# Optimization experiments

Hardware: AMD Instinct MI355X
Metric: run time of the kernel (lower is better)

Reference implementation:

```python
import jax, jax.numpy as jnp
import numpy as np

N = 50000      # nodes
E = 800000     # edges (avg degree 16)
F_IN = 512
HID = 128
OUT = 40
DROPOUT = 0.5


def setup_inputs() -> dict:
    key = jax.random.key(0)
    ks = jax.random.split(key, 9)
    x = jax.random.normal(ks[0], (N, F_IN), dtype=jnp.float32)
    edge_src = jax.random.randint(ks[1], (E,), 0, N, dtype=jnp.int32)
    edge_dst = jax.random.randint(ks[2], (E,), 0, N, dtype=jnp.int32)
    edge_weight = jax.random.uniform(ks[3], (E,), dtype=jnp.float32)
    # GraphConvolution params (Glorot-ish init like the torch reference)
    s1 = 1.0 / np.sqrt(HID)
    W1 = jax.random.uniform(ks[4], (F_IN, HID), minval=-s1, maxval=s1, dtype=jnp.float32)
    b1 = jax.random.uniform(ks[5], (HID,), minval=-s1, maxval=s1, dtype=jnp.float32)
    s2 = 1.0 / np.sqrt(OUT)
    W2 = jax.random.uniform(ks[6], (HID, OUT), minval=-s2, maxval=s2, dtype=jnp.float32)
    b2 = jax.random.uniform(ks[7], (OUT,), minval=-s2, maxval=s2, dtype=jnp.float32)
    # Pre-sampled dropout mask (training-mode dropout, deterministic reference):
    keep = jax.random.bernoulli(ks[8], 1.0 - DROPOUT, (N, HID))
    drop_mask = keep.astype(jnp.float32) / (1.0 - DROPOUT)
    return {"x": x, "W1": W1, "b1": b1, "W2": W2, "b2": b2,
            "edge_weight": edge_weight, "drop_mask": drop_mask,
            "edge_src": edge_src, "edge_dst": edge_dst}


def spmm(edge_src, edge_dst, edge_weight, h):
    # out[i] = sum_{e: dst_e = i} w_e * h[src_e]   (sparse adj @ h)
    msgs = edge_weight[:, None] * h[edge_src]      # [E, d]
    return jax.ops.segment_sum(msgs, edge_dst, num_segments=N)


def reference(x, W1, b1, W2, b2, edge_weight, drop_mask, edge_src, edge_dst):
    # layer 1: adj @ (x @ W1) + b1, relu, dropout
    h = spmm(edge_src, edge_dst, edge_weight, x @ W1) + b1
    h = jax.nn.relu(h) * drop_mask
    # layer 2: adj @ (h @ W2) + b2
    out = spmm(edge_src, edge_dst, edge_weight, h @ W2) + b2
    return out
```

## Files before the change

### kernel.cpp

```cpp
#include <hip/hip_runtime.h>

#define NN 50000
#define NE 800000
#define FIN 512
#define HID 128
#define NOUT 40
#define H2P 64
#define CAP 64
#define NXS 16
#define GB1 782
#define EPB 2048
#define SB  391
#define MB  782

typedef __bf16 v8bf __attribute__((ext_vector_type(8)));
typedef float  v4f  __attribute__((ext_vector_type(4)));
typedef unsigned short us8 __attribute__((ext_vector_type(8)));
typedef unsigned short us4 __attribute__((ext_vector_type(4)));

static __device__ __forceinline__ unsigned short f2bf(float f) {
  union { float f; unsigned int u; } v; v.f = f;
  unsigned int r = v.u + 0x7FFFu + ((v.u >> 16) & 1u);
  return (unsigned short)(r >> 16);
}
static __device__ __forceinline__ float bf2f(unsigned short s) {
  union { unsigned int u; float f; } v; v.u = ((unsigned int)s) << 16;
  return v.f;
}

__global__ void k_w1t(const float* __restrict__ W1, unsigned short* __restrict__ W1t,
                      int* __restrict__ nxt) {
  int id = blockIdx.x * 256 + threadIdx.x;
  int k = id >> 7;
  int n = id & 127;
  W1t[n * FIN + k] = f2bf(W1[k * HID + n]);
  if (id < NN) nxt[(size_t)id * NXS] = 0;
}

#define BM1 64
#define BK1 64
#define BKP1 72
__global__ __launch_bounds__(256) void k_fused(
    const float* __restrict__ x, const unsigned short* __restrict__ W1t,
    unsigned short* __restrict__ hb0,
    const int* __restrict__ src, const int* __restrict__ dst,
    const float* __restrict__ w, int* __restrict__ nxt,
    unsigned int* __restrict__ bkt,
    const float* __restrict__ mask, unsigned int* __restrict__ mpk) {
  __shared__ unsigned short As[BM1 * BKP1];
  __shared__ unsigned short Bs[HID * BKP1];
  const int t = threadIdx.x;

  if (blockIdx.x >= GB1 + SB) {
    int id = (blockIdx.x - (GB1 + SB)) * 256 + t;
    if (id < NN * 4) {
      int row = id >> 2, seg = id & 3;
      const float4* mp = (const float4*)(mask + (size_t)row * HID + seg * 32);
      unsigned int bits = 0;
      #pragma unroll
      for (int q = 0; q < 8; ++q) {
        float4 v = mp[q];
        bits |= (v.x != 0.f ? 1u : 0u) << (q * 4);
        bits |= (v.y != 0.f ? 1u : 0u) << (q * 4 + 1);
        bits |= (v.z != 0.f ? 1u : 0u) << (q * 4 + 2);
        bits |= (v.w != 0.f ? 1u : 0u) << (q * 4 + 3);
      }
      mpk[(size_t)row * 4 + seg] = bits;
    }
    return;
  }

  if (blockIdx.x >= GB1) {
    const int base = (blockIdx.x - GB1) * EPB + t;
    int   ii[8]; unsigned int pk[8]; int ok[8];
    #pragma unroll
    for (int k = 0; k < 8; ++k) {
      int e = base + k * 256;
      ok[k] = (e < NE);
      int ec = ok[k] ? e : (NE - 1);
      ii[k] = dst[ec];
      pk[k] = (unsigned int)src[ec] | ((unsigned int)f2bf(w[ec]) << 16);
    }
    int p[8];
    #pragma unroll
    for (int k = 0; k < 8; ++k)
      p[k] = ok[k] ? atomicAdd(&nxt[(size_t)ii[k] * NXS], 1) : CAP;
    #pragma unroll
    for (int k = 0; k < 8; ++k)
      if (p[k] < CAP) bkt[(size_t)ii[k] * CAP + p[k]] = pk[k];
    return;
  }

  const int r0 = blockIdx.x * BM1;
  const int wave = t >> 6, lane = t & 63;
  const int quad = lane >> 4, mr = lane & 15;
  const int mrow0 = (wave & 1) * 32;
  const int ncol0 = (wave >> 1) * 64;

  const int ar = t >> 2, aq = t & 3;
  int grow = r0 + ar; if (grow > NN - 1) grow = NN - 1;
  const float4* xrow = (const float4*)(x + (size_t)grow * FIN);
  const int bn = t >> 1, bh = t & 1;

  const v4f vzero = {0.f, 0.f, 0.f, 0.f};
  v4f acc[2][4];
  #pragma unroll
  for (int mi = 0; mi < 2; ++mi)
    #pragma unroll
    for (int j = 0; j < 4; ++j) acc[mi][j] = vzero;

  for (int k0 = 0; k0 < FIN; k0 += BK1) {
    float4 va[4];
    #pragma unroll
    for (int i = 0; i < 4; ++i) va[i] = xrow[(k0 >> 2) + aq + i * 4];
    us8 vb[4];
    const us8* bp = (const us8*)(W1t + bn * FIN + k0 + bh * 32);
    #pragma unroll
    for (int i = 0; i < 4; ++i) vb[i] = bp[i];

    __syncthreads();
    #pragma unroll
    for (int i = 0; i < 4; ++i) {
      us4 s; s.x = f2bf(va[i].x); s.y = f2bf(va[i].y);
             s.z = f2bf(va[i].z); s.w = f2bf(va[i].w);
      *(us4*)&As[ar * BKP1 + aq * 4 + i * 16] = s;
    }
    #pragma unroll
    for (int i = 0; i < 4; ++i)
      *(us8*)&Bs[bn * BKP1 + bh * 32 + i * 8] = vb[i];
    __syncthreads();

    #pragma unroll
    for (int ks = 0; ks < BK1; ks += 32) {
      v8bf a0 = *(const v8bf*)&As[(mrow0 + mr) * BKP1 + ks + quad * 8];
      v8bf a1 = *(const v8bf*)&As[(mrow0 + 16 + mr) * BKP1 + ks + quad * 8];
      #pragma unroll
      for (int j = 0; j < 4; ++j) {
        v8bf b = *(const v8bf*)&Bs[(ncol0 + j * 16 + mr) * BKP1 + ks + quad * 8];
        acc[0][j] = __builtin_amdgcn_mfma_f32_16x16x32_bf16(a0, b, acc[0][j], 0, 0, 0);
        acc[1][j] = __builtin_amdgcn_mfma_f32_16x16x32_bf16(a1, b, acc[1][j], 0, 0, 0);
      }
    }
  }

  #pragma unroll
  for (int mi = 0; mi < 2; ++mi)
    #pragma unroll
    for (int j = 0; j < 4; ++j)
      #pragma unroll
      for (int rr = 0; rr < 4; ++rr) {
        int row = r0 + mrow0 + mi * 16 + quad * 4 + rr;
        int col = ncol0 + j * 16 + mr;
        if (row < NN) hb0[(size_t)row * HID + col] = f2bf(acc[mi][j][rr]);
      }
}

__global__ __launch_bounds__(256) void k_spmm1(const unsigned short* __restrict__ hb0,
                                               const int* __restrict__ nxt,
                                               const unsigned int* __restrict__ bkt,
                                               const float* __restrict__ b1,
                                               const unsigned int* __restrict__ mpk,
                                               const float* __restrict__ W2,
                                               unsigned short* __restrict__ h2b) {
  __shared__ unsigned int w2p[64 * NOUT];
  const int t = threadIdx.x, lane = t & 63, wv = t >> 6;
  for (int idx = t; idx < 64 * NOUT; idx += 256) {
    int c2 = idx / NOUT, o = idx - c2 * NOUT;
    w2p[idx] = (unsigned int)f2bf(W2[(2 * c2) * NOUT + o])
             | ((unsigned int)f2bf(W2[(2 * c2 + 1) * NOUT + o]) << 16);
  }
  __syncthreads();

  const int g = lane >> 4, ql = lane & 15;
  const int i = blockIdx.x * 4 + wv;
  const int c0 = ql * 8;
  int nE = nxt[(size_t)i * NXS]; if (nE > CAP) nE = CAP;
  const int m = (nE + 3 - g) >> 2;
  const unsigned int* ep = bkt + (size_t)i * CAP + g;

  float a0[8] = {0.f,0.f,0.f,0.f,0.f,0.f,0.f,0.f};
  float a1[8] = {0.f,0.f,0.f,0.f,0.f,0.f,0.f,0.f};
  int j = 0;
  for (; j + 3 < m; j += 4) {
    unsigned int p0 = ep[4*j], p1 = ep[4*j+4], p2 = ep[4*j+8], p3 = ep[4*j+12];
    int s0 = p0 & 0xFFFF, s1 = p1 & 0xFFFF, s2 = p2 & 0xFFFF, s3 = p3 & 0xFFFF;
    float w0 = bf2f((unsigned short)(p0 >> 16));
    float w1 = bf2f((unsigned short)(p1 >> 16));
    float w2 = bf2f((unsigned short)(p2 >> 16));
    float w3 = bf2f((unsigned short)(p3 >> 16));
    us8 h0 = *(const us8*)&hb0[(size_t)s0 * HID + c0];
    us8 h1 = *(const us8*)&hb0[(size_t)s1 * HID + c0];
    us8 h2 = *(const us8*)&hb0[(size_t)s2 * HID + c0];
    us8 h3 = *(const us8*)&hb0[(size_t)s3 * HID + c0];
    #pragma unroll
    for (int k = 0; k < 8; ++k) {
      a0[k] += w0 * bf2f(h0[k]);
      a1[k] += w1 * bf2f(h1[k]);
      a0[k] += w2 * bf2f(h2[k]);
      a1[k] += w3 * bf2f(h3[k]);
    }
  }
  for (; j < m; ++j) {
    unsigned int p = ep[4*j];
    int s = p & 0xFFFF;
    float w = bf2f((unsigned short)(p >> 16));
    us8 h = *(const us8*)&hb0[(size_t)s * HID + c0];
    #pragma unroll
    for (int k = 0; k < 8; ++k) a0[k] += w * bf2f(h[k]);
  }
  float v[8];
  #pragma unroll
  for (int k = 0; k < 8; ++k) {
    v[k] = a0[k] + a1[k];
    v[k] += __shfl_xor(v[k], 16);
    v[k] += __shfl_xor(v[k], 32);
  }

  unsigned int word = mpk[(size_t)i * 4 + (ql >> 2)];
  unsigned int mbyte = (word >> ((ql & 3) * 8)) & 0xFFu;
  const float4 bbA = *(const float4*)&b1[c0];
  const float4 bbB = *(const float4*)&b1[c0 + 4];
  float bb[8] = {bbA.x, bbA.y, bbA.z, bbA.w, bbB.x, bbB.y, bbB.z, bbB.w};
  unsigned int rp[4];
  #pragma unroll
  for (int q = 0; q < 4; ++q) {
    float rl = ((mbyte >> (2*q))   & 1u) ? fmaxf(v[2*q]   + bb[2*q],   0.f) * 2.0f : 0.f;
    float rh = ((mbyte >> (2*q+1)) & 1u) ? fmaxf(v[2*q+1] + bb[2*q+1], 0.f) * 2.0f : 0.f;
    rp[q] = (unsigned int)f2bf(rl) | ((unsigned int)f2bf(rh) << 16);
  }

  const int o = (lane < NOUT) ? lane : (NOUT - 1);
  float acc = 0.f;
  #pragma unroll
  for (int c2 = 0; c2 < 64; ++c2) {
    unsigned int wp = w2p[c2 * NOUT + o];
    unsigned int rv = __shfl(rp[c2 & 3], c2 >> 2);
    union { unsigned int u; float f; } xl, xh, yl, yh;
    xl.u = rv << 16;  xh.u = rv & 0xFFFF0000u;
    yl.u = wp << 16;  yh.u = wp & 0xFFFF0000u;
    acc += xl.f * yl.f;
    acc += xh.f * yh.f;
  }
  float accn = __shfl_xor(acc, 1);
  if (lane < NOUT && !(lane & 1)) {
    unsigned int pk = (unsigned int)f2bf(acc) | ((unsigned int)f2bf(accn) << 16);
    *(unsigned int*)&h2b[(size_t)i * H2P + lane] = pk;
  }
}

__global__ __launch_bounds__(256) void k_spmm2(const unsigned short* __restrict__ h2b,
                                               const int* __restrict__ nxt,
                                               const unsigned int* __restrict__ bkt,
                                               const float* __restrict__ b2,
                                               float* __restrict__ out) {
  const int t = threadIdx.x, lane = t & 63;
  const int g = lane >> 4, ql = lane & 15;
  const int i = blockIdx.x * 4 + (t >> 6);
  if (i >= NN) return;
  const int act = (ql < 10);
  const int c0 = act ? ql * 4 : 0;
  int nE = nxt[(size_t)i * NXS]; if (nE > CAP) nE = CAP;
  const int m = (nE + 3 - g) >> 2;
  const unsigned int* ep = bkt + (size_t)i * CAP + g;

  float a0[4] = {0.f, 0.f, 0.f, 0.f};
  float a1[4] = {0.f, 0.f, 0.f, 0.f};
  int j = 0;
  for (; j + 3 < m; j += 4) {
    unsigned int p0 = ep[4*j], p1 = ep[4*j+4], p2 = ep[4*j+8], p3 = ep[4*j+12];
    int s0 = p0 & 0xFFFF, s1 = p1 & 0xFFFF, s2 = p2 & 0xFFFF, s3 = p3 & 0xFFFF;
    float w0 = bf2f((unsigned short)(p0 >> 16));
    float w1 = bf2f((unsigned short)(p1 >> 16));
    float w2 = bf2f((unsigned short)(p2 >> 16));
    float w3 = bf2f((unsigned short)(p3 >> 16));
    us4 h0 = *(const us4*)&h2b[(size_t)s0 * H2P + c0];
    us4 h1 = *(const us4*)&h2b[(size_t)s1 * H2P + c0];
    us4 h2 = *(const us4*)&h2b[(size_t)s2 * H2P + c0];
    us4 h3 = *(const us4*)&h2b[(size_t)s3 * H2P + c0];
    #pragma unroll
    for (int k = 0; k < 4; ++k) {
      a0[k] += w0 * bf2f(h0[k]);
      a1[k] += w1 * bf2f(h1[k]);
      a0[k] += w2 * bf2f(h2[k]);
      a1[k] += w3 * bf2f(h3[k]);
    }
  }
  for (; j < m; ++j) {
    unsigned int p = ep[4*j];
    int s = p & 0xFFFF;
    float w = bf2f((unsigned short)(p >> 16));
    us4 h = *(const us4*)&h2b[(size_t)s * H2P + c0];
    #pragma unroll
    for (int k = 0; k < 4; ++k) a0[k] += w * bf2f(h[k]);
  }
  float v[4];
  #pragma unroll
  for (int k = 0; k < 4; ++k) {
    v[k] = a0[k] + a1[k];
    v[k] += __shfl_xor(v[k], 16);
    v[k] += __shfl_xor(v[k], 32);
  }
  if (g == 0 && act) {
    const float4 bb = *(const float4*)&b2[c0];
    float4 o;
    o.x = v[0] + bb.x;
    o.y = v[1] + bb.y;
    o.z = v[2] + bb.z;
    o.w = v[3] + bb.w;
    *(float4*)&out[(size_t)i * NOUT + c0] = o;
  }
}

extern "C" void kernel_launch(void* const* d_in, const int* in_sizes, int n_in,
                              void* d_out, int out_size, void* d_ws, size_t ws_size,
                              hipStream_t stream) {
  const float* x   = (const float*)d_in[0];
  const float* W1  = (const float*)d_in[1];
  const float* b1  = (const float*)d_in[2];
  const float* W2  = (const float*)d_in[3];
  const float* b2  = (const float*)d_in[4];
  const float* ew  = (const float*)d_in[5];
  const float* msk = (const float*)d_in[6];
  const int* esrc  = (const int*)d_in[7];
  const int* edst  = (const int*)d_in[8];
  float* out = (float*)d_out;

  char* ws = (char*)d_ws;
  unsigned short* hb0 = (unsigned short*)ws; ws += (size_t)NN * HID * 2;
  unsigned short* h2b = (unsigned short*)ws; ws += (size_t)NN * H2P * 2;
  unsigned short* W1t = (unsigned short*)ws; ws += (size_t)HID * FIN * 2;
  unsigned int* bkt   = (unsigned int*)ws;   ws += (size_t)NN * CAP * 4;
  unsigned int* mpk   = (unsigned int*)ws;   ws += (size_t)NN * 4 * 4;
  int* nxt            = (int*)ws;            ws += (size_t)NN * NXS * 4;

  k_w1t  <<<(FIN * HID) / 256, 256, 0, stream>>>(W1, W1t, nxt);
  k_fused<<<GB1 + SB + MB, 256, 0, stream>>>(x, W1t, hb0,
                                             esrc, edst, ew, nxt, bkt,
                                             msk, mpk);
  k_spmm1<<<NN / 4, 256, 0, stream>>>(hb0, nxt, bkt, b1, mpk, W2, h2b);
  k_spmm2<<<(NN + 3) / 4, 256, 0, stream>>>(h2b, nxt, bkt, b2, out);
}
```

Before: 324.9 us.

## Split layer-2 matmul out of spmm1 into MFMA GEMM kernel; pack FMAs

Removes the per-row scalar h@W2 product (with W2 repacked into LDS by every block) from the first SpMM kernel. The SpMM now writes the post-ReLU/dropout hidden activations to a new bf16 buffer, and a separate kernel multiplies them by W2 with bf16 MFMA, padding the 40 output columns to 48. Both SpMM inner loops also switch to two-wide float vectors so the compiler can emit packed FMAs. In exchange it adds an extra kernel launch and a write and reread of the 50000x128 bf16 intermediate.

```diff
diff --git a/kernel.cpp b/kernel.cpp
--- a/kernel.cpp
+++ b/kernel.cpp
@@ -15,8 +15,11 @@
 
 typedef __bf16 v8bf __attribute__((ext_vector_type(8)));
 typedef float  v4f  __attribute__((ext_vector_type(4)));
+typedef float  v2f  __attribute__((ext_vector_type(2)));
 typedef unsigned short us8 __attribute__((ext_vector_type(8)));
 typedef unsigned short us4 __attribute__((ext_vector_type(4)));
+typedef unsigned int   u32x4 __attribute__((ext_vector_type(4)));
+typedef unsigned int   u32x2 __attribute__((ext_vector_type(2)));
 
 static __device__ __forceinline__ unsigned short f2bf(float f) {
   union { float f; unsigned int u; } v; v.f = f;
@@ -26,6 +29,13 @@
 static __device__ __forceinline__ float bf2f(unsigned short s) {
   union { unsigned int u; float f; } v; v.u = ((unsigned int)s) << 16;
   return v.f;
+}
+static __device__ __forceinline__ float u2f(unsigned int u) {
+  union { unsigned int u; float f; } v; v.u = u;
+  return v.f;
+}
+static __device__ __forceinline__ v2f bfp2f(unsigned int u) {
+  v2f r; r.x = u2f(u << 16); r.y = u2f(u & 0xFFFF0000u); return r;
 }
 
 __global__ void k_w1t(const float* __restrict__ W1, unsigned short* __restrict__ W1t,
@@ -160,17 +170,8 @@
                                                const unsigned int* __restrict__ bkt,
                                                const float* __restrict__ b1,
                                                const unsigned int* __restrict__ mpk,
-                                               const float* __restrict__ W2,
-                                               unsigned short* __restrict__ h2b) {
-  __shared__ unsigned int w2p[64 * NOUT];
+                                               unsigned short* __restrict__ hb1) {
   const int t = threadIdx.x, lane = t & 63, wv = t >> 6;
-  for (int idx = t; idx < 64 * NOUT; idx += 256) {
-    int c2 = idx / NOUT, o = idx - c2 * NOUT;
-    w2p[idx] = (unsigned int)f2bf(W2[(2 * c2) * NOUT + o])
-             | ((unsigned int)f2bf(W2[(2 * c2 + 1) * NOUT + o]) << 16);
-  }
-  __syncthreads();
-
   const int g = lane >> 4, ql = lane & 15;
   const int i = blockIdx.x * 4 + wv;
   const int c0 = ql * 8;
@@ -178,74 +179,115 @@
   const int m = (nE + 3 - g) >> 2;
   const unsigned int* ep = bkt + (size_t)i * CAP + g;
 
-  float a0[8] = {0.f,0.f,0.f,0.f,0.f,0.f,0.f,0.f};
-  float a1[8] = {0.f,0.f,0.f,0.f,0.f,0.f,0.f,0.f};
+  const v2f z2 = {0.f, 0.f};
+  v2f a0p[4] = {z2, z2, z2, z2};
+  v2f a1p[4] = {z2, z2, z2, z2};
   int j = 0;
   for (; j + 3 < m; j += 4) {
     unsigned int p0 = ep[4*j], p1 = ep[4*j+4], p2 = ep[4*j+8], p3 = ep[4*j+12];
     int s0 = p0 & 0xFFFF, s1 = p1 & 0xFFFF, s2 = p2 & 0xFFFF, s3 = p3 & 0xFFFF;
-    float w0 = bf2f((unsigned short)(p0 >> 16));
-    float w1 = bf2f((unsigned short)(p1 >> 16));
-    float w2 = bf2f((unsigned short)(p2 >> 16));
-    float w3 = bf2f((unsigned short)(p3 >> 16));
-    us8 h0 = *(const us8*)&hb0[(size_t)s0 * HID + c0];
-    us8 h1 = *(const us8*)&hb0[(size_t)s1 * HID + c0];
-    us8 h2 = *(const us8*)&hb0[(size_t)s2 * HID + c0];
-    us8 h3 = *(const us8*)&hb0[(size_t)s3 * HID + c0];
-    #pragma unroll
-    for (int k = 0; k < 8; ++k) {
-      a0[k] += w0 * bf2f(h0[k]);
-      a1[k] += w1 * bf2f(h1[k]);
-      a0[k] += w2 * bf2f(h2[k]);
-      a1[k] += w3 * bf2f(h3[k]);
+    v2f w0 = {0.f, 0.f}, w1 = w0, w2 = w0, w3 = w0;
+    w0.x = w0.y = bf2f((unsigned short)(p0 >> 16));
+    w1.x = w1.y = bf2f((unsigned short)(p1 >> 16));
+    w2.x = w2.y = bf2f((unsigned short)(p2 >> 16));
+    w3.x = w3.y = bf2f((unsigned short)(p3 >> 16));
+    u32x4 h0 = *(const u32x4*)&hb0[(size_t)s0 * HID + c0];
+    u32x4 h1 = *(const u32x4*)&hb0[(size_t)s1 * HID + c0];
+    u32x4 h2 = *(const u32x4*)&hb0[(size_t)s2 * HID + c0];
+    u32x4 h3 = *(const u32x4*)&hb0[(size_t)s3 * HID + c0];
+    #pragma unroll
+    for (int d = 0; d < 4; ++d) {
+      a0p[d] += w0 * bfp2f(h0[d]);
+      a1p[d] += w1 * bfp2f(h1[d]);
+      a0p[d] += w2 * bfp2f(h2[d]);
+      a1p[d] += w3 * bfp2f(h3[d]);
     }
   }
   for (; j < m; ++j) {
     unsigned int p = ep[4*j];
     int s = p & 0xFFFF;
-    float w = bf2f((unsigned short)(p >> 16));
-    us8 h = *(const us8*)&hb0[(size_t)s * HID + c0];
-    #pragma unroll
-    for (int k = 0; k < 8; ++k) a0[k] += w * bf2f(h[k]);
+    v2f w; w.x = w.y = bf2f((unsigned short)(p >> 16));
+    u32x4 h = *(const u32x4*)&hb0[(size_t)s * HID + c0];
+    #pragma unroll
+    for (int d = 0; d < 4; ++d) a0p[d] += w * bfp2f(h[d]);
   }
   float v[8];
   #pragma unroll
+  for (int d = 0; d < 4; ++d) {
+    v2f s = a0p[d] + a1p[d];
+    v[2*d] = s.x; v[2*d+1] = s.y;
+  }
+  #pragma unroll
   for (int k = 0; k < 8; ++k) {
-    v[k] = a0[k] + a1[k];
     v[k] += __shfl_xor(v[k], 16);
     v[k] += __shfl_xor(v[k], 32);
   }
-
-  unsigned int word = mpk[(size_t)i * 4 + (ql >> 2)];
-  unsigned int mbyte = (word >> ((ql & 3) * 8)) & 0xFFu;
-  const float4 bbA = *(const float4*)&b1[c0];
-  const float4 bbB = *(const float4*)&b1[c0 + 4];
-  float bb[8] = {bbA.x, bbA.y, bbA.z, bbA.w, bbB.x, bbB.y, bbB.z, bbB.w};
-  unsigned int rp[4];
-  #pragma unroll
-  for (int q = 0; q < 4; ++q) {
-    float rl = ((mbyte >> (2*q))   & 1u) ? fmaxf(v[2*q]   + bb[2*q],   0.f) * 2.0f : 0.f;
-    float rh = ((mbyte >> (2*q+1)) & 1u) ? fmaxf(v[2*q+1] + bb[2*q+1], 0.f) * 2.0f : 0.f;
-    rp[q] = (unsigned int)f2bf(rl) | ((unsigned int)f2bf(rh) << 16);
-  }
-
-  const int o = (lane < NOUT) ? lane : (NOUT - 1);
-  float acc = 0.f;
-  #pragma unroll
-  for (int c2 = 0; c2 < 64; ++c2) {
-    unsigned int wp = w2p[c2 * NOUT + o];
-    unsigned int rv = __shfl(rp[c2 & 3], c2 >> 2);
-    union { unsigned int u; float f; } xl, xh, yl, yh;
-    xl.u = rv << 16;  xh.u = rv & 0xFFFF0000u;
-    yl.u = wp << 16;  yh.u = wp & 0xFFFF0000u;
-    acc += xl.f * yl.f;
-    acc += xh.f * yh.f;
-  }
-  float accn = __shfl_xor(acc, 1);
-  if (lane < NOUT && !(lane & 1)) {
-    unsigned int pk = (unsigned int)f2bf(acc) | ((unsigned int)f2bf(accn) << 16);
-    *(unsigned int*)&h2b[(size_t)i * H2P + lane] = pk;
-  }
+  if (g == 0) {
+    unsigned int word = mpk[(size_t)i * 4 + (ql >> 2)];
+    unsigned int byte = (word >> ((ql & 3) * 8)) & 0xFFu;
+    const float4 bbA = *(const float4*)&b1[c0];
+    const float4 bbB = *(const float4*)&b1[c0 + 4];
+    float bb[8] = {bbA.x, bbA.y, bbA.z, bbA.w, bbB.x, bbB.y, bbB.z, bbB.w};
+    us8 o;
+    #pragma unroll
+    for (int k = 0; k < 8; ++k) {
+      float r = ((byte >> k) & 1u) ? fmaxf(v[k] + bb[k], 0.f) * 2.0f : 0.f;
+      o[k] = f2bf(r);
+    }
+    *(us8*)&hb1[(size_t)i * HID + c0] = o;
+  }
+}
+
+#define BKP2 136
+__global__ __launch_bounds__(256) void k_gemm2(const unsigned short* __restrict__ hb1,
+                                               const float* __restrict__ W2,
+                                               unsigned short* __restrict__ h2b) {
+  __shared__ unsigned short As[64 * BKP2];
+  __shared__ unsigned short Bs[48 * BKP2];
+  const int t = threadIdx.x;
+  const int r0 = blockIdx.x * 64;
+  const int wave = t >> 6, lane = t & 63;
+  const int quad = lane >> 4, mr = lane & 15;
+  const int mrow0 = wave * 16;
+
+  const int ar = t >> 2, aq = t & 3;
+  int grow = r0 + ar; if (grow > NN - 1) grow = NN - 1;
+  const us8* hrow = (const us8*)(hb1 + (size_t)grow * HID);
+  #pragma unroll
+  for (int i = 0; i < 4; ++i) {
+    us8 v = hrow[aq + i * 4];
+    *(us8*)&As[ar * BKP2 + aq * 8 + i * 32] = v;
+  }
+  if (t < 192) {
+    int n = t >> 2, q = t & 3;
+    #pragma unroll
+    for (int kk = 0; kk < 32; ++kk) {
+      int k = q * 32 + kk;
+      float val = (n < NOUT) ? W2[k * NOUT + n] : 0.f;
+      Bs[n * BKP2 + k] = f2bf(val);
+    }
+  }
+  __syncthreads();
+
+  const v4f vzero = {0.f, 0.f, 0.f, 0.f};
+  v4f acc[3] = {vzero, vzero, vzero};
+  #pragma unroll
+  for (int ks = 0; ks < HID; ks += 32) {
+    v8bf a = *(const v8bf*)&As[(mrow0 + mr) * BKP2 + ks + quad * 8];
+    #pragma unroll
+    for (int j = 0; j < 3; ++j) {
+      v8bf b = *(const v8bf*)&Bs[(j * 16 + mr) * BKP2 + ks + quad * 8];
+      acc[j] = __builtin_amdgcn_mfma_f32_16x16x32_bf16(a, b, acc[j], 0, 0, 0);
+    }
+  }
+  #pragma unroll
+  for (int j = 0; j < 3; ++j)
+    #pragma unroll
+    for (int rr = 0; rr < 4; ++rr) {
+      int row = r0 + mrow0 + quad * 4 + rr;
+      int col = j * 16 + mr;
+      if (row < NN && col < NOUT) h2b[(size_t)row * H2P + col] = f2bf(acc[j][rr]);
+    }
 }
 
 __global__ __launch_bounds__(256) void k_spmm2(const unsigned short* __restrict__ h2b,
@@ -263,40 +305,46 @@
   const int m = (nE + 3 - g) >> 2;
   const unsigned int* ep = bkt + (size_t)i * CAP + g;
 
-  float a0[4] = {0.f, 0.f, 0.f, 0.f};
-  float a1[4] = {0.f, 0.f, 0.f, 0.f};
+  const v2f z2 = {0.f, 0.f};
+  v2f a0p[2] = {z2, z2};
+  v2f a1p[2] = {z2, z2};
   int j = 0;
   for (; j + 3 < m; j += 4) {
     unsigned int p0 = ep[4*j], p1 = ep[4*j+4], p2 = ep[4*j+8], p3 = ep[4*j+12];
     int s0 = p0 & 0xFFFF, s1 = p1 & 0xFFFF, s2 = p2 & 0xFFFF, s3 = p3 & 0xFFFF;
-    float w0 = bf2f((unsigned short)(p0 >> 16));
-    float w1 = bf2f((unsigned short)(p1 >> 16));
-    float w2 = bf2f((unsigned short)(p2 >> 16));
-    float w3 = bf2f((unsigned short)(p3 >> 16));
-    us4 h0 = *(const us4*)&h2b[(size_t)s0 * H2P + c0];
-    us4 h1 = *(const us4*)&h2b[(size_t)s1 * H2P + c0];
-    us4 h2 = *(const us4*)&h2b[(size_t)s2 * H2P + c0];
-    us4 h3 = *(const us4*)&h2b[(size_t)s3 * H2P + c0];
-    #pragma unroll
-    for (int k = 0; k < 4; ++k) {
-      a0[k] += w0 * bf2f(h0[k]);
-      a1[k] += w1 * bf2f(h1[k]);
-      a0[k] += w2 * bf2f(h2[k]);
-      a1[k] += w3 * bf2f(h3[k]);
+    v2f w0, w1, w2, w3;
+    w0.x = w0.y = bf2f((unsigned short)(p0 >> 16));
+    w1.x = w1.y = bf2f((unsigned short)(p1 >> 16));
+    w2.x = w2.y = bf2f((unsigned short)(p2 >> 16));
+    w3.x = w3.y = bf2f((unsigned short)(p3 >> 16));
+    u32x2 h0 = *(const u32x2*)&h2b[(size_t)s0 * H2P + c0];
+    u32x2 h1 = *(const u32x2*)&h2b[(size_t)s1 * H2P + c0];
+    u32x2 h2 = *(const u32x2*)&h2b[(size_t)s2 * H2P + c0];
+    u32x2 h3 = *(const u32x2*)&h2b[(size_t)s3 * H2P + c0];
+    #pragma unroll
+    for (int d = 0; d < 2; ++d) {
+      a0p[d] += w0 * bfp2f(h0[d]);
+      a1p[d] += w1 * bfp2f(h1[d]);
+      a0p[d] += w2 * bfp2f(h2[d]);
+      a1p[d] += w3 * bfp2f(h3[d]);
     }
   }
   for (; j < m; ++j) {
     unsigned int p = ep[4*j];
     int s = p & 0xFFFF;
-    float w = bf2f((unsigned short)(p >> 16));
-    us4 h = *(const us4*)&h2b[(size_t)s * H2P + c0];
-    #pragma unroll
-    for (int k = 0; k < 4; ++k) a0[k] += w * bf2f(h[k]);
+    v2f w; w.x = w.y = bf2f((unsigned short)(p >> 16));
+    u32x2 h = *(const u32x2*)&h2b[(size_t)s * H2P + c0];
+    #pragma unroll
+    for (int d = 0; d < 2; ++d) a0p[d] += w * bfp2f(h[d]);
   }
   float v[4];
   #pragma unroll
+  for (int d = 0; d < 2; ++d) {
+    v2f s = a0p[d] + a1p[d];
+    v[2*d] = s.x; v[2*d+1] = s.y;
+  }
+  #pragma unroll
   for (int k = 0; k < 4; ++k) {
-    v[k] = a0[k] + a1[k];
     v[k] += __shfl_xor(v[k], 16);
     v[k] += __shfl_xor(v[k], 32);
   }
@@ -327,6 +375,7 @@
 
   char* ws = (char*)d_ws;
   unsigned short* hb0 = (unsigned short*)ws; ws += (size_t)NN * HID * 2;
+  unsigned short* hb1 = (unsigned short*)ws; ws += (size_t)NN * HID * 2;
   unsigned short* h2b = (unsigned short*)ws; ws += (size_t)NN * H2P * 2;
   unsigned short* W1t = (unsigned short*)ws; ws += (size_t)HID * FIN * 2;
   unsigned int* bkt   = (unsigned int*)ws;   ws += (size_t)NN * CAP * 4;
@@ -337,6 +386,7 @@
   k_fused<<<GB1 + SB + MB, 256, 0, stream>>>(x, W1t, hb0,
                                              esrc, edst, ew, nxt, bkt,
                                              msk, mpk);
-  k_spmm1<<<NN / 4, 256, 0, stream>>>(hb0, nxt, bkt, b1, mpk, W2, h2b);
+  k_spmm1<<<NN / 4, 256, 0, stream>>>(hb0, nxt, bkt, b1, mpk, hb1);
+  k_gemm2<<<(NN + 63) / 64, 256, 0, stream>>>(hb1, W2, h2b);
   k_spmm2<<<(NN + 3) / 4, 256, 0, stream>>>(h2b, nxt, bkt, b2, out);
 }
```

New measurement: 295.4 us. -9.1%, faster.
